# Kernel tuning notes

Measured on AMD Instinct MI355X. Metric: run time of the kernel, lower is better.

## Reference

```python
import jax, jax.numpy as jnp
import numpy as np

B, S, D_MODEL, HEADS = 4, 2048, 1024, 16
D_HEAD = D_MODEL // HEADS  # 64


def setup_inputs() -> dict:
    key = jax.random.key(0)
    ks = jax.random.split(key, 10)
    scale = 1.0 / np.sqrt(D_MODEL)
    return {
        "query": jax.random.normal(ks[0], (B, S, D_MODEL), dtype=jnp.float32),
        "key_": jax.random.normal(ks[1], (B, S, D_MODEL), dtype=jnp.float32),
        "value": jax.random.normal(ks[2], (B, S, D_MODEL), dtype=jnp.float32),
        "mask": jax.random.randint(ks[3], (B, S, S), 0, 2).astype(bool),
        "Wq": jax.random.normal(ks[4], (D_MODEL, HEADS, D_HEAD), dtype=jnp.float32) * scale,
        "bq": jnp.zeros((HEADS, D_HEAD), dtype=jnp.float32),
        "Wk": jax.random.normal(ks[5], (D_MODEL, HEADS, D_HEAD), dtype=jnp.float32) * scale,
        "bk": jnp.zeros((HEADS, D_HEAD), dtype=jnp.float32),
        "Wv": jax.random.normal(ks[6], (D_MODEL, HEADS, D_HEAD), dtype=jnp.float32) * scale,
        "bv": jnp.zeros((HEADS, D_HEAD), dtype=jnp.float32),
        "Wo": jax.random.normal(ks[7], (HEADS, D_HEAD, D_MODEL), dtype=jnp.float32) * (1.0 / np.sqrt(D_MODEL)),
        "bo": jnp.zeros((D_MODEL,), dtype=jnp.float32),
    }


def reference(query, key_, value, mask, Wq, bq, Wk, bk, Wv, bv, Wo, bo):
    # MakeHead: linear projection to (B, heads, S, d_head)
    q = jnp.einsum("bse,ehd->bhsd", query, Wq) + bq[:, None, :]
    k = jnp.einsum("bse,ehd->bhsd", key_, Wk) + bk[:, None, :]
    v = jnp.einsum("bse,ehd->bhsd", value, Wv) + bv[:, None, :]

    # dot_product_attention (note: module divides by sqrt(d_head) AFTER softmax@V)
    logits = jnp.einsum("bhsd,bhtd->bhst", q, k)  # [B,H,S,S]
    logits = jnp.where(mask[:, None, :, :], jnp.float32(-1e8), logits)
    score = jax.nn.softmax(logits, axis=-1)
    attn = jnp.einsum("bhst,bhtd->bhsd", score, v) / jnp.sqrt(jnp.float32(D_HEAD))

    # MergeHeads: project back to d_output = d_model
    out = jnp.einsum("bhsd,hdo->bso", attn, Wo) + bo
    return out
```

## Files before the change

kernel.cpp:

```cpp
#include <hip/hip_runtime.h>

typedef _Float16 h16;
typedef h16 half8 __attribute__((ext_vector_type(8)));
typedef h16 half4v __attribute__((ext_vector_type(4)));
typedef float f32x4 __attribute__((ext_vector_type(4)));

#define BB 4
#define SS 2048
#define EE 1024
#define HH 16
#define DH 64

__device__ __forceinline__ void gload_lds16(const void* g, void* l) {
  __builtin_amdgcn_global_load_lds((const __attribute__((address_space(1))) void*)g,
                                   (__attribute__((address_space(3))) void*)l, 16, 0, 0);
}

__global__ __launch_bounds__(256) void mha_pack_mask(const int* __restrict__ mask,
                                                     unsigned* __restrict__ maskw) {
  int gid = blockIdx.x * 256 + threadIdx.x;
  unsigned long long bal = __ballot(mask[gid] != 0);
  int lane = threadIdx.x & 63;
  if (lane == 0) maskw[gid >> 5] = (unsigned)bal;
  else if (lane == 32) maskw[gid >> 5] = (unsigned)(bal >> 32);
}

__global__ __launch_bounds__(256) void mha_wtrans(const float* __restrict__ w0, const float* __restrict__ w1,
                                                  const float* __restrict__ w2, const float* __restrict__ w3,
                                                  h16* __restrict__ o0, h16* __restrict__ o1,
                                                  h16* __restrict__ o2, h16* __restrict__ o3) {
  __shared__ float t[32][33];
  int z = blockIdx.z;
  const float* src = z == 0 ? w0 : z == 1 ? w1 : z == 2 ? w2 : w3;
  h16* dst = z == 0 ? o0 : z == 1 ? o1 : z == 2 ? o2 : o3;
  int x = threadIdx.x, y = threadIdx.y;
  int bx = blockIdx.x * 32, by = blockIdx.y * 32;
#pragma unroll
  for (int i = 0; i < 4; ++i)
    t[y + i * 8][x] = src[(size_t)(by + y + i * 8) * EE + bx + x];
  __syncthreads();
#pragma unroll
  for (int i = 0; i < 4; ++i)
    dst[(size_t)(bx + y + i * 8) * EE + by + x] = (h16)t[x][y + i * 8];
}

__global__ __launch_bounds__(256) void mha_cvt(const float* __restrict__ s0, const float* __restrict__ s1,
                                               const float* __restrict__ s2, h16* __restrict__ d0,
                                               h16* __restrict__ d1, h16* __restrict__ d2) {
  int z = blockIdx.z;
  const float* s = z == 0 ? s0 : z == 1 ? s1 : s2;
  h16* d = z == 0 ? d0 : z == 1 ? d1 : d2;
  size_t i = ((size_t)blockIdx.x * 256 + threadIdx.x) * 8;
  float4 a = *reinterpret_cast<const float4*>(&s[i]);
  float4 b = *reinterpret_cast<const float4*>(&s[i + 4]);
  half8 h;
  h[0] = (h16)a.x; h[1] = (h16)a.y; h[2] = (h16)a.z; h[3] = (h16)a.w;
  h[4] = (h16)b.x; h[5] = (h16)b.y; h[6] = (h16)b.z; h[7] = (h16)b.w;
  *reinterpret_cast<half8*>(&d[i]) = h;
}

#define PTM 128
#define PTN 128
#define PBK 32

__global__ __launch_bounds__(256) void mha_proj(
    const h16* __restrict__ Xq, const h16* __restrict__ Xk, const h16* __restrict__ Xv,
    const h16* __restrict__ Wqt, const h16* __restrict__ Wkt, const h16* __restrict__ Wvt,
    const float* __restrict__ bq, const float* __restrict__ bk, const float* __restrict__ bv,
    h16* __restrict__ Oq, h16* __restrict__ Ok, h16* __restrict__ Ov) {
  int z = blockIdx.z;
  const h16* X = z == 0 ? Xq : z == 1 ? Xk : Xv;
  const h16* Wt = z == 0 ? Wqt : z == 1 ? Wkt : Wvt;
  const float* bias = z == 0 ? bq : z == 1 ? bk : bv;
  h16* out = z == 0 ? Oq : z == 1 ? Ok : Ov;

  __shared__ __align__(16) h16 As[PTM * PBK];
  __shared__ __align__(16) h16 Bs[PTN * PBK];

  int tid = threadIdx.x;
  int lane = tid & 63, wid = tid >> 6;
  int l15 = lane & 15, l4 = lane >> 4;
  int wr = wid >> 1, wc = wid & 1;
  int mbase = blockIdx.y * PTM;
  int nbase = blockIdx.x * PTN;

  const f32x4 fz = {0.f, 0.f, 0.f, 0.f};
  f32x4 acc[4][4];
#pragma unroll
  for (int i = 0; i < 4; ++i)
#pragma unroll
    for (int j = 0; j < 4; ++j) acc[i][j] = fz;

  int row0 = wid * 32 + (lane >> 2), chunk = lane & 3;

  for (int kt = 0; kt < EE; kt += PBK) {
#pragma unroll
    for (int c = 0; c < 2; ++c) {
      int r = row0 + c * 16;
      gload_lds16(&X[(size_t)(mbase + r) * EE + kt + chunk * 8], &As[wid * 1024 + c * 512]);
      gload_lds16(&Wt[(size_t)(nbase + r) * EE + kt + chunk * 8], &Bs[wid * 1024 + c * 512]);
    }
    __syncthreads();

    half8 a[4], bfr[4];
#pragma unroll
    for (int i = 0; i < 4; ++i) {
      a[i] = *reinterpret_cast<const half8*>(&As[(wr * 64 + i * 16 + l15) * PBK + l4 * 8]);
      bfr[i] = *reinterpret_cast<const half8*>(&Bs[(wc * 64 + i * 16 + l15) * PBK + l4 * 8]);
    }
#pragma unroll
    for (int mi = 0; mi < 4; ++mi)
#pragma unroll
      for (int ni = 0; ni < 4; ++ni)
        acc[mi][ni] = __builtin_amdgcn_mfma_f32_16x16x32_f16(a[mi], bfr[ni], acc[mi][ni], 0, 0, 0);
    __syncthreads();
  }

  const float qscale = (z == 0) ? 1.44269504088896f : 1.0f;
#pragma unroll
  for (int mi = 0; mi < 4; ++mi) {
#pragma unroll
    for (int ni = 0; ni < 4; ++ni) {
      int n = nbase + wc * 64 + ni * 16 + l15;
      float bv_ = bias[n];
      int h = n >> 6, d = n & 63;
#pragma unroll
      for (int j = 0; j < 4; ++j) {
        int m = mbase + wr * 64 + mi * 16 + l4 * 4 + j;
        int b_ = m >> 11, s = m & 2047;
        h16 hv = (h16)((acc[mi][ni][j] + bv_) * qscale);
        if (z != 2)
          out[(((size_t)(b_ * HH + h)) * SS + s) * DH + d] = hv;
        else
          out[(((size_t)(b_ * HH + h)) * DH + d) * SS + s] = hv;
      }
    }
  }
}

__global__ __launch_bounds__(256) void mha_attn(
    const h16* __restrict__ qh, const h16* __restrict__ kh, const h16* __restrict__ vh,
    const unsigned* __restrict__ maskw, h16* __restrict__ ah) {
  __shared__ __align__(16) h16 Ks[2][64 * 64];
  __shared__ __align__(16) h16 Vs[2][64 * 64];

  int bh = blockIdx.y;
  int b_ = bh >> 4, hh = bh & 15;
  int tid = threadIdx.x, lane = tid & 63, wid = tid >> 6;
  int l15 = lane & 15, l4 = lane >> 4;

  const h16* Qb = qh + (size_t)bh * SS * DH;
  const h16* Kb = kh + (size_t)bh * SS * DH;
  const h16* Vb = vh + (size_t)bh * DH * SS;
  int qrow0 = blockIdx.x * 128 + wid * 32;

  half8 qf[2][2];
#pragma unroll
  for (int mi = 0; mi < 2; ++mi)
#pragma unroll
    for (int kk = 0; kk < 2; ++kk)
      qf[mi][kk] = *reinterpret_cast<const half8*>(&Qb[(size_t)(qrow0 + mi * 16 + l15) * DH + kk * 32 + l4 * 8]);

  float m_run[2] = {-1e30f, -1e30f};
  f32x4 l_vec[2];
  f32x4 oacc[2][4];
  const f32x4 fz = {0.f, 0.f, 0.f, 0.f};
#pragma unroll
  for (int mi = 0; mi < 2; ++mi) {
    l_vec[mi] = fz;
#pragma unroll
    for (int di = 0; di < 4; ++di) oacc[mi][di] = fz;
  }

  const unsigned* mwb = maskw + ((size_t)b_ * SS + qrow0) * 64;

  int srow = wid * 16 + (lane >> 3);
  int schunk = lane & 7;
  int sh0 = l4 * 8;

#pragma unroll
  for (int c = 0; c < 2; ++c) {
    int rp = srow + c * 8;
    int rl = (rp & 32) + ((rp >> 2) & 3) * 8 + ((rp >> 4) & 1) * 4 + (rp & 3);
    int gk = schunk ^ (rp & 7);
    gload_lds16(&Kb[(size_t)rl * DH + gk * 8], &Ks[0][wid * 1024 + c * 512]);
    gload_lds16(&Vb[(size_t)rp * SS + gk * 8], &Vs[0][wid * 1024 + c * 512]);
  }
  unsigned mw[2][2];
  mw[0][0] = mwb[l15 * 64 + 0];
  mw[0][1] = mwb[l15 * 64 + 1];
  mw[1][0] = mwb[(16 + l15) * 64 + 0];
  mw[1][1] = mwb[(16 + l15) * 64 + 1];
  __syncthreads();

  const unsigned negb = __float_as_uint(-1e5f);

  int it = 0;
  for (int tt = 0; tt < SS; tt += 64, it ^= 1) {
    unsigned mwn[2][2] = {{0u, 0u}, {0u, 0u}};
    if (tt + 64 < SS) {
#pragma unroll
      for (int c = 0; c < 2; ++c) {
        int rp = srow + c * 8;
        int rl = (rp & 32) + ((rp >> 2) & 3) * 8 + ((rp >> 4) & 1) * 4 + (rp & 3);
        int gk = schunk ^ (rp & 7);
        gload_lds16(&Kb[(size_t)(tt + 64 + rl) * DH + gk * 8], &Ks[it ^ 1][wid * 1024 + c * 512]);
        gload_lds16(&Vb[(size_t)rp * SS + tt + 64 + gk * 8], &Vs[it ^ 1][wid * 1024 + c * 512]);
      }
      int tw = (tt + 64) >> 5;
      mwn[0][0] = mwb[l15 * 64 + tw];
      mwn[0][1] = mwb[l15 * 64 + tw + 1];
      mwn[1][0] = mwb[(16 + l15) * 64 + tw];
      mwn[1][1] = mwb[(16 + l15) * 64 + tw + 1];
    }

    const h16* Kt = &Ks[it][0];
    half8 kf[4][2];
#pragma unroll
    for (int ni = 0; ni < 4; ++ni) {
      int trow = ni * 16 + l15;
      int sw = trow & 7;
      kf[ni][0] = *reinterpret_cast<const half8*>(&Kt[trow * 64 + (l4 ^ sw) * 8]);
      kf[ni][1] = *reinterpret_cast<const half8*>(&Kt[trow * 64 + ((4 + l4) ^ sw) * 8]);
    }
    f32x4 st[2][4];
    __builtin_amdgcn_s_setprio(1);
#pragma unroll
    for (int mi = 0; mi < 2; ++mi)
#pragma unroll
      for (int ni = 0; ni < 4; ++ni) {
        f32x4 t_ = fz;
        t_ = __builtin_amdgcn_mfma_f32_16x16x32_f16(kf[ni][0], qf[mi][0], t_, 0, 0, 0);
        t_ = __builtin_amdgcn_mfma_f32_16x16x32_f16(kf[ni][1], qf[mi][1], t_, 0, 0, 0);
        st[mi][ni] = t_;
      }
    __builtin_amdgcn_s_setprio(0);

    const h16* Vt = &Vs[it][0];
    half8 vf[4][2];
#pragma unroll
    for (int di = 0; di < 4; ++di) {
      int dr = di * 16 + l15, sw = dr & 7;
#pragma unroll
      for (int kb = 0; kb < 2; ++kb) {
        int ch = (kb * 4 + l4) ^ sw;
        vf[di][kb] = *reinterpret_cast<const half8*>(&Vt[dr * 64 + ch * 8]);
      }
    }

#pragma unroll
    for (int mi = 0; mi < 2; ++mi) {
#pragma unroll
      for (int ni = 0; ni < 4; ++ni) {
        unsigned m4 = mw[mi][ni >> 1] >> (sh0 + 4 * (ni & 1));
#pragma unroll
        for (int j = 0; j < 4; ++j) {
          unsigned sel = (unsigned)(((int)(m4 << (31 - j))) >> 31);
          st[mi][ni][j] = __uint_as_float((~sel & __float_as_uint(st[mi][ni][j])) | (sel & negb));
        }
      }
    }

    half8 pfrag[2][2];
#pragma unroll
    for (int mi = 0; mi < 2; ++mi) {
      float t0 = fmaxf(fmaxf(st[mi][0][0], st[mi][0][1]), st[mi][0][2]);
      float t1 = fmaxf(fmaxf(st[mi][0][3], st[mi][1][0]), st[mi][1][1]);
      float t2 = fmaxf(fmaxf(st[mi][1][2], st[mi][1][3]), st[mi][2][0]);
      float t3 = fmaxf(fmaxf(st[mi][2][1], st[mi][2][2]), st[mi][2][3]);
      float t4 = fmaxf(fmaxf(st[mi][3][0], st[mi][3][1]), st[mi][3][2]);
      float tmax = fmaxf(fmaxf(fmaxf(t0, t1), fmaxf(t2, t3)), fmaxf(t4, st[mi][3][3]));
      tmax = fmaxf(tmax, __shfl_xor(tmax, 16));
      tmax = fmaxf(tmax, __shfl_xor(tmax, 32));
      if (!__all(tmax - m_run[mi] <= 8.0f)) {
        float mnew = fmaxf(m_run[mi], tmax);
        float sc = __builtin_amdgcn_exp2f(m_run[mi] - mnew);
        l_vec[mi] *= sc;
#pragma unroll
        for (int di = 0; di < 4; ++di) oacc[mi][di] *= sc;
        m_run[mi] = mnew;
      }
      float mneg = -m_run[mi];
#pragma unroll
      for (int ni = 0; ni < 4; ++ni)
#pragma unroll
        for (int j = 0; j < 4; ++j)
          st[mi][ni][j] = __builtin_amdgcn_exp2f(st[mi][ni][j] + mneg);
      l_vec[mi] += (st[mi][0] + st[mi][1]) + (st[mi][2] + st[mi][3]);
#pragma unroll
      for (int kb = 0; kb < 2; ++kb) {
        auto pa = __builtin_amdgcn_cvt_pkrtz(st[mi][2 * kb][0], st[mi][2 * kb][1]);
        auto pb = __builtin_amdgcn_cvt_pkrtz(st[mi][2 * kb][2], st[mi][2 * kb][3]);
        auto pc = __builtin_amdgcn_cvt_pkrtz(st[mi][2 * kb + 1][0], st[mi][2 * kb + 1][1]);
        auto pd = __builtin_amdgcn_cvt_pkrtz(st[mi][2 * kb + 1][2], st[mi][2 * kb + 1][3]);
        pfrag[mi][kb][0] = pa[0]; pfrag[mi][kb][1] = pa[1];
        pfrag[mi][kb][2] = pb[0]; pfrag[mi][kb][3] = pb[1];
        pfrag[mi][kb][4] = pc[0]; pfrag[mi][kb][5] = pc[1];
        pfrag[mi][kb][6] = pd[0]; pfrag[mi][kb][7] = pd[1];
      }
    }

    __builtin_amdgcn_s_setprio(1);
#pragma unroll
    for (int mi = 0; mi < 2; ++mi)
#pragma unroll
      for (int di = 0; di < 4; ++di) {
        oacc[mi][di] = __builtin_amdgcn_mfma_f32_16x16x32_f16(vf[di][0], pfrag[mi][0], oacc[mi][di], 0, 0, 0);
        oacc[mi][di] = __builtin_amdgcn_mfma_f32_16x16x32_f16(vf[di][1], pfrag[mi][1], oacc[mi][di], 0, 0, 0);
      }
    __builtin_amdgcn_s_setprio(0);

    mw[0][0] = mwn[0][0]; mw[0][1] = mwn[0][1];
    mw[1][0] = mwn[1][0]; mw[1][1] = mwn[1][1];
    __syncthreads();
  }

#pragma unroll
  for (int mi = 0; mi < 2; ++mi) {
    float l = (l_vec[mi][0] + l_vec[mi][1]) + (l_vec[mi][2] + l_vec[mi][3]);
    l += __shfl_xor(l, 16);
    l += __shfl_xor(l, 32);
    float inv = 1.f / (l * 8.f);
    size_t rowb = ((size_t)b_ * SS + (qrow0 + mi * 16 + l15)) * EE + hh * DH;
#pragma unroll
    for (int di = 0; di < 4; ++di) {
      half4v w;
#pragma unroll
      for (int j = 0; j < 4; ++j) w[j] = (h16)(oacc[mi][di][j] * inv);
      *reinterpret_cast<half4v*>(&ah[rowb + di * 16 + l4 * 4]) = w;
    }
  }
}

__global__ __launch_bounds__(256) void mha_oproj(
    const h16* __restrict__ A, const h16* __restrict__ Wot,
    const float* __restrict__ bo, float* __restrict__ out) {
  __shared__ __align__(16) h16 As[PTM * PBK];
  __shared__ __align__(16) h16 Bs[PTN * PBK];
  int tid = threadIdx.x, lane = tid & 63, wid = tid >> 6;
  int l15 = lane & 15, l4 = lane >> 4;
  int wr = wid >> 1, wc = wid & 1;
  int mbase = blockIdx.y * PTM, nbase = blockIdx.x * PTN;
  const f32x4 fz = {0.f, 0.f, 0.f, 0.f};
  f32x4 acc[4][4];
#pragma unroll
  for (int i = 0; i < 4; ++i)
#pragma unroll
    for (int j = 0; j < 4; ++j) acc[i][j] = fz;
  int row0 = wid * 32 + (lane >> 2), chunk = lane & 3;
  for (int kt = 0; kt < EE; kt += PBK) {
#pragma unroll
    for (int c = 0; c < 2; ++c) {
      int r = row0 + c * 16;
      gload_lds16(&A[(size_t)(mbase + r) * EE + kt + chunk * 8], &As[wid * 1024 + c * 512]);
      gload_lds16(&Wot[(size_t)(nbase + r) * EE + kt + chunk * 8], &Bs[wid * 1024 + c * 512]);
    }
    __syncthreads();
    half8 a[4], bfr[4];
#pragma unroll
    for (int i = 0; i < 4; ++i) {
      a[i] = *reinterpret_cast<const half8*>(&As[(wr * 64 + i * 16 + l15) * PBK + l4 * 8]);
      bfr[i] = *reinterpret_cast<const half8*>(&Bs[(wc * 64 + i * 16 + l15) * PBK + l4 * 8]);
    }
#pragma unroll
    for (int mi = 0; mi < 4; ++mi)
#pragma unroll
      for (int ni = 0; ni < 4; ++ni)
        acc[mi][ni] = __builtin_amdgcn_mfma_f32_16x16x32_f16(a[mi], bfr[ni], acc[mi][ni], 0, 0, 0);
    __syncthreads();
  }
#pragma unroll
  for (int mi = 0; mi < 4; ++mi)
#pragma unroll
    for (int ni = 0; ni < 4; ++ni) {
      int n = nbase + wc * 64 + ni * 16 + l15;
      float bb = bo[n];
#pragma unroll
      for (int j = 0; j < 4; ++j) {
        int m = mbase + wr * 64 + mi * 16 + l4 * 4 + j;
        out[(size_t)m * EE + n] = acc[mi][ni][j] + bb;
      }
    }
}

extern "C" void kernel_launch(void* const* d_in, const int* in_sizes, int n_in,
                              void* d_out, int out_size, void* d_ws, size_t ws_size,
                              hipStream_t stream) {
  const float* query = (const float*)d_in[0];
  const float* key_ = (const float*)d_in[1];
  const float* value = (const float*)d_in[2];
  const int* mask = (const int*)d_in[3];
  const float* Wq = (const float*)d_in[4];
  const float* bq = (const float*)d_in[5];
  const float* Wk = (const float*)d_in[6];
  const float* bk = (const float*)d_in[7];
  const float* Wv = (const float*)d_in[8];
  const float* bv = (const float*)d_in[9];
  const float* Wo = (const float*)d_in[10];
  const float* bo = (const float*)d_in[11];
  float* out = (float*)d_out;

  const size_t MH = 1u << 20;
  const size_t QH = (size_t)BB * HH * SS * DH;
  h16* wqt = (h16*)d_ws;
  h16* wkt = wqt + MH;
  h16* wvt = wkt + MH;
  h16* wot = wvt + MH;
  h16* qh = wot + MH;
  h16* kh = qh + QH;
  h16* vh = kh + QH;
  h16* ah = vh + QH;
  unsigned* maskw = (unsigned*)(ah + QH);

  h16* xq = ah;
  h16* xk = (h16*)d_out;
  h16* xv = xk + QH;

  mha_pack_mask<<<(BB * SS * SS) / 256, 256, 0, stream>>>(mask, maskw);
  mha_wtrans<<<dim3(32, 32, 4), dim3(32, 8), 0, stream>>>(Wq, Wk, Wv, Wo, wqt, wkt, wvt, wot);
  mha_cvt<<<dim3((BB * SS * EE) / 2048, 1, 3), 256, 0, stream>>>(query, key_, value, xq, xk, xv);
  mha_proj<<<dim3(EE / PTN, (BB * SS) / PTM, 3), 256, 0, stream>>>(
      xq, xk, xv, wqt, wkt, wvt, bq, bk, bv, qh, kh, vh);
  mha_attn<<<dim3(SS / 128, BB * HH), 256, 0, stream>>>(qh, kh, vh, maskw, ah);
  mha_oproj<<<dim3(EE / PTN, (BB * SS) / PTM), 256, 0, stream>>>(ah, wot, bo, out);
}
```

Measured before the change: 327.6 us.

## Double GEMM K-tile with XOR-swizzled LDS, MFMA row sums in attention

The projection and output GEMMs now use a 64-wide K tile. Their LDS tiles are stored with an XOR swizzle, which halves the number of barrier-separated iterations and avoids LDS bank conflicts on fragment reads. In the attention kernel, the softmax denominator is accumulated with an extra MFMA against a ones vector instead of VALU adds and cross-lane shuffles, and the K/V pointer arithmetic is hoisted out of the loop. This trades extra matrix-core work and doubled LDS per block for fewer vector instructions and barriers.

```diff
diff --git a/kernel.cpp b/kernel.cpp
--- a/kernel.cpp
+++ b/kernel.cpp
@@ -61,7 +61,7 @@
 
 #define PTM 128
 #define PTN 128
-#define PBK 32
+#define PBK 64
 
 __global__ __launch_bounds__(256) void mha_proj(
     const h16* __restrict__ Xq, const h16* __restrict__ Xk, const h16* __restrict__ Xv,
@@ -91,28 +91,37 @@
 #pragma unroll
     for (int j = 0; j < 4; ++j) acc[i][j] = fz;
 
-  int row0 = wid * 32 + (lane >> 2), chunk = lane & 3;
+  int r_loc = lane >> 3;
+  int ch = lane & 7;
 
   for (int kt = 0; kt < EE; kt += PBK) {
 #pragma unroll
-    for (int c = 0; c < 2; ++c) {
-      int r = row0 + c * 16;
-      gload_lds16(&X[(size_t)(mbase + r) * EE + kt + chunk * 8], &As[wid * 1024 + c * 512]);
-      gload_lds16(&Wt[(size_t)(nbase + r) * EE + kt + chunk * 8], &Bs[wid * 1024 + c * 512]);
+    for (int c = 0; c < 4; ++c) {
+      int row = c * 32 + wid * 8 + r_loc;
+      int sc_ = ch ^ (row & 7);
+      gload_lds16(&X[(size_t)(mbase + row) * EE + kt + sc_ * 8], &As[(c * 32 + wid * 8) * PBK]);
+      gload_lds16(&Wt[(size_t)(nbase + row) * EE + kt + sc_ * 8], &Bs[(c * 32 + wid * 8) * PBK]);
     }
     __syncthreads();
 
-    half8 a[4], bfr[4];
+    half8 a[2][4], b[2][4];
 #pragma unroll
     for (int i = 0; i < 4; ++i) {
-      a[i] = *reinterpret_cast<const half8*>(&As[(wr * 64 + i * 16 + l15) * PBK + l4 * 8]);
-      bfr[i] = *reinterpret_cast<const half8*>(&Bs[(wc * 64 + i * 16 + l15) * PBK + l4 * 8]);
-    }
-#pragma unroll
-    for (int mi = 0; mi < 4; ++mi)
-#pragma unroll
-      for (int ni = 0; ni < 4; ++ni)
-        acc[mi][ni] = __builtin_amdgcn_mfma_f32_16x16x32_f16(a[mi], bfr[ni], acc[mi][ni], 0, 0, 0);
+      int ra = wr * 64 + i * 16 + l15;
+      int rb = wc * 64 + i * 16 + l15;
+#pragma unroll
+      for (int kk = 0; kk < 2; ++kk) {
+        a[kk][i] = *reinterpret_cast<const half8*>(&As[ra * PBK + ((kk * 4 + l4) ^ (ra & 7)) * 8]);
+        b[kk][i] = *reinterpret_cast<const half8*>(&Bs[rb * PBK + ((kk * 4 + l4) ^ (rb & 7)) * 8]);
+      }
+    }
+#pragma unroll
+    for (int kk = 0; kk < 2; ++kk)
+#pragma unroll
+      for (int mi = 0; mi < 4; ++mi)
+#pragma unroll
+        for (int ni = 0; ni < 4; ++ni)
+          acc[mi][ni] = __builtin_amdgcn_mfma_f32_16x16x32_f16(a[kk][mi], b[kk][ni], acc[mi][ni], 0, 0, 0);
     __syncthreads();
   }
 
@@ -161,13 +170,17 @@
     for (int kk = 0; kk < 2; ++kk)
       qf[mi][kk] = *reinterpret_cast<const half8*>(&Qb[(size_t)(qrow0 + mi * 16 + l15) * DH + kk * 32 + l4 * 8]);
 
+  half8 ones;
+#pragma unroll
+  for (int e = 0; e < 8; ++e) ones[e] = (h16)1.0f;
+
   float m_run[2] = {-1e30f, -1e30f};
-  f32x4 l_vec[2];
+  f32x4 l_acc[2];
   f32x4 oacc[2][4];
   const f32x4 fz = {0.f, 0.f, 0.f, 0.f};
 #pragma unroll
   for (int mi = 0; mi < 2; ++mi) {
-    l_vec[mi] = fz;
+    l_acc[mi] = fz;
 #pragma unroll
     for (int di = 0; di < 4; ++di) oacc[mi][di] = fz;
   }
@@ -178,14 +191,19 @@
   int schunk = lane & 7;
   int sh0 = l4 * 8;
 
-#pragma unroll
-  for (int c = 0; c < 2; ++c) {
-    int rp = srow + c * 8;
-    int rl = (rp & 32) + ((rp >> 2) & 3) * 8 + ((rp >> 4) & 1) * 4 + (rp & 3);
-    int gk = schunk ^ (rp & 7);
-    gload_lds16(&Kb[(size_t)rl * DH + gk * 8], &Ks[0][wid * 1024 + c * 512]);
-    gload_lds16(&Vb[(size_t)rp * SS + gk * 8], &Vs[0][wid * 1024 + c * 512]);
-  }
+  int rp0 = srow, rp1 = srow + 8;
+  int rl0 = (rp0 & 32) + ((rp0 >> 2) & 3) * 8 + ((rp0 >> 4) & 1) * 4 + (rp0 & 3);
+  int rl1 = (rp1 & 32) + ((rp1 >> 2) & 3) * 8 + ((rp1 >> 4) & 1) * 4 + (rp1 & 3);
+  int gk0 = schunk ^ (rp0 & 7), gk1 = schunk ^ (rp1 & 7);
+  const h16* kp0 = Kb + (size_t)rl0 * DH + gk0 * 8;
+  const h16* kp1 = Kb + (size_t)rl1 * DH + gk1 * 8;
+  const h16* vp0 = Vb + (size_t)rp0 * SS + gk0 * 8;
+  const h16* vp1 = Vb + (size_t)rp1 * SS + gk1 * 8;
+
+  gload_lds16(kp0, &Ks[0][wid * 1024]);
+  gload_lds16(vp0, &Vs[0][wid * 1024]);
+  gload_lds16(kp1, &Ks[0][wid * 1024 + 512]);
+  gload_lds16(vp1, &Vs[0][wid * 1024 + 512]);
   unsigned mw[2][2];
   mw[0][0] = mwb[l15 * 64 + 0];
   mw[0][1] = mwb[l15 * 64 + 1];
@@ -199,14 +217,11 @@
   for (int tt = 0; tt < SS; tt += 64, it ^= 1) {
     unsigned mwn[2][2] = {{0u, 0u}, {0u, 0u}};
     if (tt + 64 < SS) {
-#pragma unroll
-      for (int c = 0; c < 2; ++c) {
-        int rp = srow + c * 8;
-        int rl = (rp & 32) + ((rp >> 2) & 3) * 8 + ((rp >> 4) & 1) * 4 + (rp & 3);
-        int gk = schunk ^ (rp & 7);
-        gload_lds16(&Kb[(size_t)(tt + 64 + rl) * DH + gk * 8], &Ks[it ^ 1][wid * 1024 + c * 512]);
-        gload_lds16(&Vb[(size_t)rp * SS + tt + 64 + gk * 8], &Vs[it ^ 1][wid * 1024 + c * 512]);
-      }
+      size_t ko = (size_t)(tt + 64) * DH;
+      gload_lds16(kp0 + ko, &Ks[it ^ 1][wid * 1024]);
+      gload_lds16(vp0 + tt + 64, &Vs[it ^ 1][wid * 1024]);
+      gload_lds16(kp1 + ko, &Ks[it ^ 1][wid * 1024 + 512]);
+      gload_lds16(vp1 + tt + 64, &Vs[it ^ 1][wid * 1024 + 512]);
       int tw = (tt + 64) >> 5;
       mwn[0][0] = mwb[l15 * 64 + tw];
       mwn[0][1] = mwb[l15 * 64 + tw + 1];
@@ -275,7 +290,7 @@
       if (!__all(tmax - m_run[mi] <= 8.0f)) {
         float mnew = fmaxf(m_run[mi], tmax);
         float sc = __builtin_amdgcn_exp2f(m_run[mi] - mnew);
-        l_vec[mi] *= sc;
+        l_acc[mi][0] *= sc;
 #pragma unroll
         for (int di = 0; di < 4; ++di) oacc[mi][di] *= sc;
         m_run[mi] = mnew;
@@ -286,7 +301,6 @@
 #pragma unroll
         for (int j = 0; j < 4; ++j)
           st[mi][ni][j] = __builtin_amdgcn_exp2f(st[mi][ni][j] + mneg);
-      l_vec[mi] += (st[mi][0] + st[mi][1]) + (st[mi][2] + st[mi][3]);
 #pragma unroll
       for (int kb = 0; kb < 2; ++kb) {
         auto pa = __builtin_amdgcn_cvt_pkrtz(st[mi][2 * kb][0], st[mi][2 * kb][1]);
@@ -302,12 +316,15 @@
 
     __builtin_amdgcn_s_setprio(1);
 #pragma unroll
-    for (int mi = 0; mi < 2; ++mi)
+    for (int mi = 0; mi < 2; ++mi) {
 #pragma unroll
       for (int di = 0; di < 4; ++di) {
         oacc[mi][di] = __builtin_amdgcn_mfma_f32_16x16x32_f16(vf[di][0], pfrag[mi][0], oacc[mi][di], 0, 0, 0);
         oacc[mi][di] = __builtin_amdgcn_mfma_f32_16x16x32_f16(vf[di][1], pfrag[mi][1], oacc[mi][di], 0, 0, 0);
       }
+      l_acc[mi] = __builtin_amdgcn_mfma_f32_16x16x32_f16(ones, pfrag[mi][0], l_acc[mi], 0, 0, 0);
+      l_acc[mi] = __builtin_amdgcn_mfma_f32_16x16x32_f16(ones, pfrag[mi][1], l_acc[mi], 0, 0, 0);
+    }
     __builtin_amdgcn_s_setprio(0);
 
     mw[0][0] = mwn[0][0]; mw[0][1] = mwn[0][1];
@@ -317,10 +334,7 @@
 
 #pragma unroll
   for (int mi = 0; mi < 2; ++mi) {
-    float l = (l_vec[mi][0] + l_vec[mi][1]) + (l_vec[mi][2] + l_vec[mi][3]);
-    l += __shfl_xor(l, 16);
-    l += __shfl_xor(l, 32);
-    float inv = 1.f / (l * 8.f);
+    float inv = 1.f / (l_acc[mi][0] * 8.f);
     size_t rowb = ((size_t)b_ * SS + (qrow0 + mi * 16 + l15)) * EE + hh * DH;
 #pragma unroll
     for (int di = 0; di < 4; ++di) {
@@ -347,26 +361,36 @@
   for (int i = 0; i < 4; ++i)
 #pragma unroll
     for (int j = 0; j < 4; ++j) acc[i][j] = fz;
-  int row0 = wid * 32 + (lane >> 2), chunk = lane & 3;
+
+  int r_loc = lane >> 3, ch = lane & 7;
+
   for (int kt = 0; kt < EE; kt += PBK) {
 #pragma unroll
-    for (int c = 0; c < 2; ++c) {
-      int r = row0 + c * 16;
-      gload_lds16(&A[(size_t)(mbase + r) * EE + kt + chunk * 8], &As[wid * 1024 + c * 512]);
-      gload_lds16(&Wot[(size_t)(nbase + r) * EE + kt + chunk * 8], &Bs[wid * 1024 + c * 512]);
+    for (int c = 0; c < 4; ++c) {
+      int row = c * 32 + wid * 8 + r_loc;
+      int sc_ = ch ^ (row & 7);
+      gload_lds16(&A[(size_t)(mbase + row) * EE + kt + sc_ * 8], &As[(c * 32 + wid * 8) * PBK]);
+      gload_lds16(&Wot[(size_t)(nbase + row) * EE + kt + sc_ * 8], &Bs[(c * 32 + wid * 8) * PBK]);
     }
     __syncthreads();
-    half8 a[4], bfr[4];
+    half8 a[2][4], b[2][4];
 #pragma unroll
     for (int i = 0; i < 4; ++i) {
-      a[i] = *reinterpret_cast<const half8*>(&As[(wr * 64 + i * 16 + l15) * PBK + l4 * 8]);
-      bfr[i] = *reinterpret_cast<const half8*>(&Bs[(wc * 64 + i * 16 + l15) * PBK + l4 * 8]);
-    }
-#pragma unroll
-    for (int mi = 0; mi < 4; ++mi)
-#pragma unroll
-      for (int ni = 0; ni < 4; ++ni)
-        acc[mi][ni] = __builtin_amdgcn_mfma_f32_16x16x32_f16(a[mi], bfr[ni], acc[mi][ni], 0, 0, 0);
+      int ra = wr * 64 + i * 16 + l15;
+      int rb = wc * 64 + i * 16 + l15;
+#pragma unroll
+      for (int kk = 0; kk < 2; ++kk) {
+        a[kk][i] = *reinterpret_cast<const half8*>(&As[ra * PBK + ((kk * 4 + l4) ^ (ra & 7)) * 8]);
+        b[kk][i] = *reinterpret_cast<const half8*>(&Bs[rb * PBK + ((kk * 4 + l4) ^ (rb & 7)) * 8]);
+      }
+    }
+#pragma unroll
+    for (int kk = 0; kk < 2; ++kk)
+#pragma unroll
+      for (int mi = 0; mi < 4; ++mi)
+#pragma unroll
+        for (int ni = 0; ni < 4; ++ni)
+          acc[mi][ni] = __builtin_amdgcn_mfma_f32_16x16x32_f16(a[kk][mi], b[kk][ni], acc[mi][ni], 0, 0, 0);
     __syncthreads();
   }
 #pragma unroll
```

Measured after the change: 323.3 us. No clear change (-1.3%).
